# Kernel optimization log

Hardware: AMD Instinct MI355X
Metric: run time of the kernel (lower is better)

The kernel has to match this reference:

```python
import jax, jax.numpy as jnp
import numpy as np

B, S, C = 16, 2048, 256      # batch, seq_len, in_channels
QK, H = 256, 8               # qk_dim, num_heads
N, ED = 512, 256             # envbook_num+1, envbook_dim
D = QK // H                  # per_head_dim
SCALING = QK ** (-0.5)       # note: original scales by full qk_dim, not per-head dim


def setup_inputs() -> dict:
    key = jax.random.key(0)
    k1, k2, k3, k4 = jax.random.split(key, 4)
    x = jax.random.normal(k1, (B, S, C), dtype=jnp.float32)
    env_codebook = jax.random.normal(k2, (N, ED), dtype=jnp.float32)
    # nn.Linear weights stored transposed for x @ W convention
    Wq = jax.random.normal(k3, (C, QK), dtype=jnp.float32) * (1.0 / np.sqrt(C))
    Wk = jax.random.normal(k4, (ED, QK), dtype=jnp.float32) * (1.0 / np.sqrt(ED))
    return {"x": x, "env_codebook": env_codebook, "Wq": Wq, "Wk": Wk}


def reference(x, env_codebook, Wq, Wk):
    # query: [B,S,QK] -> [B,S,H,D]; key: [N,QK] -> [N,H,D]
    q = (x @ Wq).reshape(B, S, H, D)
    k = (env_codebook @ Wk).reshape(N, H, D)
    # scores: [B,H,S,N]
    scores = jnp.einsum("bshd,nhd->bhsn", q, k) * SCALING
    probs = jax.nn.softmax(scores, axis=-1)
    causal_att = probs[..., 0]          # [B,H,S]
    env_selects = probs[..., 1:]        # [B,H,S,N-1]
    env_att = env_selects.sum(axis=-1)  # [B,H,S]
    return (env_att, causal_att, env_selects)
```

## Files before the change

### kernel.cpp

```cpp
#include <hip/hip_runtime.h>
#include <hip/hip_bf16.h>

#define B_  16
#define S_  2048
#define C_  256
#define QK_ 256
#define H_  8
#define N_  512
#define D_  32

typedef short  bf16x8 __attribute__((ext_vector_type(8)));
typedef float  f32x4  __attribute__((ext_vector_type(4)));

__device__ __forceinline__ unsigned short f2bf(float f) {
    union { float f; unsigned u; } v; v.f = f;
    unsigned r = v.u + 0x7fffu + ((v.u >> 16) & 1u);
    return (unsigned short)(r >> 16);
}

__global__ void k_prep(const float* __restrict__ Wq,
                       const float* __restrict__ env,
                       const float* __restrict__ Wk,
                       unsigned short* __restrict__ wqt,
                       unsigned short* __restrict__ kbf) {
    __shared__ float erow[256];
    int bid = blockIdx.x, t = threadIdx.x;
    if (bid < 256) {
        wqt[bid * 256 + t] = f2bf(Wq[t * 256 + bid]);
    } else {
        int n = bid - 256;
        erow[t] = env[n * 256 + t];
        __syncthreads();
        float acc = 0.f;
#pragma unroll 8
        for (int c = 0; c < 256; ++c) acc += erow[c] * Wk[c * 256 + t];
        int h = t >> 5, d = t & 31;
        kbf[(h * N_ + n) * D_ + d] = f2bf(acc);
    }
}

__global__ __launch_bounds__(256) void k_qproj(
        const float* __restrict__ x,
        const unsigned short* __restrict__ wqt,
        unsigned short* __restrict__ qws) {
    int tid  = threadIdx.x;
    int lane = tid & 63, w = tid >> 6;
    int l15  = lane & 15, quad = lane >> 4;
    int r0   = blockIdx.x * 16;
    int nb   = w * 64;

    const float* arow = x + (size_t)(r0 + l15) * 256 + quad * 8;
    const unsigned short* brow[4];
#pragma unroll
    for (int nt = 0; nt < 4; ++nt)
        brow[nt] = wqt + (size_t)(nb + nt * 16 + l15) * 256 + quad * 8;

    f32x4 acc[4] = {};
#pragma unroll
    for (int kk = 0; kk < 8; ++kk) {
        float4 f0 = *(const float4*)(arow + kk * 32);
        float4 f1 = *(const float4*)(arow + kk * 32 + 4);
        bf16x8 a;
        a[0] = (short)f2bf(f0.x); a[1] = (short)f2bf(f0.y);
        a[2] = (short)f2bf(f0.z); a[3] = (short)f2bf(f0.w);
        a[4] = (short)f2bf(f1.x); a[5] = (short)f2bf(f1.y);
        a[6] = (short)f2bf(f1.z); a[7] = (short)f2bf(f1.w);
#pragma unroll
        for (int nt = 0; nt < 4; ++nt) {
            bf16x8 b = *(const bf16x8*)(brow[nt] + kk * 32);
            acc[nt] = __builtin_amdgcn_mfma_f32_16x16x32_bf16(a, b, acc[nt], 0, 0, 0);
        }
    }
#pragma unroll
    for (int nt = 0; nt < 4; ++nt) {
        int col = nb + nt * 16 + l15;
        int h = col >> 5, d = col & 31;
#pragma unroll
        for (int r = 0; r < 4; ++r) {
            int gr = r0 + quad * 4 + r;
            int b = gr >> 11, s = gr & 2047;
            qws[(((size_t)(b * H_ + h)) * S_ + s) * D_ + d] = f2bf(acc[nt][r] * 0.0625f);
        }
    }
}

#define PADW 514
__global__ __launch_bounds__(256) void k_scores(
        const unsigned short* __restrict__ qws,
        const unsigned short* __restrict__ kbf,
        float* __restrict__ out) {
    float* env_att = out;
    float* causal  = out + (size_t)B_ * H_ * S_;
    float* es      = out + (size_t)2 * B_ * H_ * S_;

    __shared__ float red[4][16];
    __shared__ float tile[16 * PADW];

    int tid  = threadIdx.x;
    int lane = tid & 63, w = tid >> 6;
    int l15  = lane & 15, quad = lane >> 4;

    int bid  = blockIdx.x;
    int bh   = bid >> 4;
    int sblk = (bid & 15) * 128;
    int h    = bh & 7;

    const unsigned short* kb = kbf + (size_t)h * N_ * D_;
    int nb = w * 128;
    bf16x8 bf[8];
#pragma unroll
    for (int j = 0; j < 8; ++j)
        bf[j] = *(const bf16x8*)(kb + (size_t)(nb + j * 16 + l15) * D_ + quad * 8);

    const unsigned short* qbase = qws + (size_t)bh * S_ * D_;

    for (int st = 0; st < 8; ++st) {
        int s0 = sblk + st * 16;
        bf16x8 a = *(const bf16x8*)(qbase + (size_t)(s0 + l15) * D_ + quad * 8);

        f32x4 c[8];
#pragma unroll
        for (int j = 0; j < 8; ++j) {
            f32x4 z = {};
            c[j] = __builtin_amdgcn_mfma_f32_16x16x32_bf16(a, bf[j], z, 0, 0, 0);
        }
        float psum[4] = {0.f, 0.f, 0.f, 0.f};
#pragma unroll
        for (int j = 0; j < 8; ++j)
#pragma unroll
            for (int r = 0; r < 4; ++r) {
                float e = __expf(c[j][r]);
                c[j][r] = e;
                psum[r] += e;
            }
#pragma unroll
        for (int off = 1; off < 16; off <<= 1)
#pragma unroll
            for (int r = 0; r < 4; ++r)
                psum[r] += __shfl_xor(psum[r], off, 64);
        if (l15 == 0) {
#pragma unroll
            for (int r = 0; r < 4; ++r) red[w][quad * 4 + r] = psum[r];
        }
        __syncthreads();
        float inv[4];
#pragma unroll
        for (int r = 0; r < 4; ++r) {
            int row = quad * 4 + r;
            float tot = red[0][row] + red[1][row] + red[2][row] + red[3][row];
            inv[r] = 1.0f / tot;
        }
#pragma unroll
        for (int j = 0; j < 8; ++j) {
            int n = nb + j * 16 + l15;
#pragma unroll
            for (int r = 0; r < 4; ++r)
                tile[(quad * 4 + r) * PADW + n] = c[j][r] * inv[r];
        }
        if (w == 0 && l15 == 0) {
            int srow = bh * S_ + s0 + quad * 4;
#pragma unroll
            for (int r = 0; r < 4; ++r) {
                float p0 = c[0][r] * inv[r];
                causal[srow + r]  = p0;
                env_att[srow + r] = 1.0f - p0;
            }
        }
        __syncthreads();
        size_t region = ((size_t)bh * S_ + s0) * 511;
#pragma unroll
        for (int row = 0; row < 16; ++row) {
            es[region + row * 511 + tid] = tile[row * PADW + 1 + tid];
            if (tid < 255)
                es[region + row * 511 + 256 + tid] = tile[row * PADW + 257 + tid];
        }
    }
}

extern "C" void kernel_launch(void* const* d_in, const int* in_sizes, int n_in,
                              void* d_out, int out_size, void* d_ws, size_t ws_size,
                              hipStream_t stream) {
    const float* x   = (const float*)d_in[0];
    const float* env = (const float*)d_in[1];
    const float* Wq  = (const float*)d_in[2];
    const float* Wk  = (const float*)d_in[3];
    float* out = (float*)d_out;

    char* ws = (char*)d_ws;
    unsigned short* qws = (unsigned short*)(ws);
    unsigned short* kbf = (unsigned short*)(ws + 16777216);
    unsigned short* wqt = (unsigned short*)(ws + 17039360);

    k_prep  <<<768,  256, 0, stream>>>(Wq, env, Wk, wqt, kbf);
    k_qproj <<<2048, 256, 0, stream>>>(x, wqt, qws);
    k_scores<<<2048, 256, 0, stream>>>(qws, kbf, out);
}
```

Measured before the change: 634.2 us.

## Vectorize env_selects stores with nontemporal float4 writes and defer normalization

Restructures the scores kernel epilogue. Unnormalized exp values go into a shifted LDS tile so that each thread can read a float4 row segment, scale it by the reciprocal of the row sum, and write it back with nontemporal vector stores. The row-sum exchange is folded into the two existing barriers, and the next Q fragment is prefetched during the store phase. This cuts scalar global stores and one sync pass, but the stores are only 4-byte aligned because rows are 511 floats long, and the fast rcp is slightly less accurate.

```diff
diff --git a/kernel.cpp b/kernel.cpp
--- a/kernel.cpp
+++ b/kernel.cpp
@@ -11,11 +11,17 @@
 
 typedef short  bf16x8 __attribute__((ext_vector_type(8)));
 typedef float  f32x4  __attribute__((ext_vector_type(4)));
+typedef float  f32x4u __attribute__((ext_vector_type(4), aligned(4)));
 
 __device__ __forceinline__ unsigned short f2bf(float f) {
     union { float f; unsigned u; } v; v.f = f;
     unsigned r = v.u + 0x7fffu + ((v.u >> 16) & 1u);
     return (unsigned short)(r >> 16);
+}
+
+__device__ __forceinline__ void bar_lgkm() {
+    asm volatile("s_waitcnt lgkmcnt(0)" ::: "memory");
+    __builtin_amdgcn_s_barrier();
 }
 
 __global__ void k_prep(const float* __restrict__ Wq,
@@ -84,7 +90,7 @@
     }
 }
 
-#define PADW 514
+#define PADW2 516
 __global__ __launch_bounds__(256) void k_scores(
         const unsigned short* __restrict__ qws,
         const unsigned short* __restrict__ kbf,
@@ -94,7 +100,8 @@
     float* es      = out + (size_t)2 * B_ * H_ * S_;
 
     __shared__ float red[4][16];
-    __shared__ float tile[16 * PADW];
+    __shared__ float p0v[16];
+    __shared__ float tile[16 * PADW2];
 
     int tid  = threadIdx.x;
     int lane = tid & 63, w = tid >> 6;
@@ -113,10 +120,10 @@
         bf[j] = *(const bf16x8*)(kb + (size_t)(nb + j * 16 + l15) * D_ + quad * 8);
 
     const unsigned short* qbase = qws + (size_t)bh * S_ * D_;
+    bf16x8 a = *(const bf16x8*)(qbase + (size_t)(sblk + l15) * D_ + quad * 8);
 
     for (int st = 0; st < 8; ++st) {
         int s0 = sblk + st * 16;
-        bf16x8 a = *(const bf16x8*)(qbase + (size_t)(s0 + l15) * D_ + quad * 8);
 
         f32x4 c[8];
 #pragma unroll
@@ -138,41 +145,55 @@
 #pragma unroll
             for (int r = 0; r < 4; ++r)
                 psum[r] += __shfl_xor(psum[r], off, 64);
-        if (l15 == 0) {
-#pragma unroll
-            for (int r = 0; r < 4; ++r) red[w][quad * 4 + r] = psum[r];
-        }
-        __syncthreads();
-        float inv[4];
-#pragma unroll
-        for (int r = 0; r < 4; ++r) {
-            int row = quad * 4 + r;
-            float tot = red[0][row] + red[1][row] + red[2][row] + red[3][row];
-            inv[r] = 1.0f / tot;
-        }
+
+        bar_lgkm();
+
 #pragma unroll
         for (int j = 0; j < 8; ++j) {
             int n = nb + j * 16 + l15;
 #pragma unroll
             for (int r = 0; r < 4; ++r)
-                tile[(quad * 4 + r) * PADW + n] = c[j][r] * inv[r];
+                if (n != 0) tile[(quad * 4 + r) * PADW2 + (n - 1)] = c[j][r];
+        }
+        if (l15 == 0) {
+#pragma unroll
+            for (int r = 0; r < 4; ++r) red[w][quad * 4 + r] = psum[r];
         }
         if (w == 0 && l15 == 0) {
-            int srow = bh * S_ + s0 + quad * 4;
-#pragma unroll
-            for (int r = 0; r < 4; ++r) {
-                float p0 = c[0][r] * inv[r];
-                causal[srow + r]  = p0;
-                env_att[srow + r] = 1.0f - p0;
+#pragma unroll
+            for (int r = 0; r < 4; ++r) p0v[quad * 4 + r] = c[0][r];
+        }
+
+        bar_lgkm();
+
+        if (st < 7)
+            a = *(const bf16x8*)(qbase + (size_t)(s0 + 16 + l15) * D_ + quad * 8);
+
+        size_t region = ((size_t)bh * S_ + s0) * 511;
+        int t    = tid & 127;
+        int rsel = tid >> 7;
+#pragma unroll
+        for (int rp = 0; rp < 8; ++rp) {
+            int row = rp * 2 + rsel;
+            float tot = red[0][row] + red[1][row] + red[2][row] + red[3][row];
+            float inv = __builtin_amdgcn_rcpf(tot);
+            f32x4 v = *(const f32x4*)&tile[row * PADW2 + 4 * t];
+            v *= inv;
+            float* dst = es + region + (size_t)row * 511 + 4 * t;
+            if (t < 127) {
+                __builtin_nontemporal_store((f32x4u)v, (f32x4u*)dst);
+            } else {
+                __builtin_nontemporal_store(v.x, dst);
+                __builtin_nontemporal_store(v.y, dst + 1);
+                __builtin_nontemporal_store(v.z, dst + 2);
             }
         }
-        __syncthreads();
-        size_t region = ((size_t)bh * S_ + s0) * 511;
-#pragma unroll
-        for (int row = 0; row < 16; ++row) {
-            es[region + row * 511 + tid] = tile[row * PADW + 1 + tid];
-            if (tid < 255)
-                es[region + row * 511 + 256 + tid] = tile[row * PADW + 257 + tid];
+        if (tid < 16) {
+            float tot = red[0][tid] + red[1][tid] + red[2][tid] + red[3][tid];
+            float p0  = p0v[tid] * __builtin_amdgcn_rcpf(tot);
+            int srow  = bh * S_ + s0 + tid;
+            causal[srow]  = p0;
+            env_att[srow] = 1.0f - p0;
         }
     }
 }
```

Result: no change. 641.9 us (+1.2%).
